# Kernel tuning notes

Measured on AMD Instinct MI355X. Metric: run time of the kernel, lower is better.

## Reference

```python
import jax, jax.numpy as jnp
import numpy as np

H = 2            # attention heads
HID = 128        # hidden_channels
NEG_SLOPE = 0.2  # GATConv leaky_relu slope

N_USER, N_POST, N_ENT = 100000, 50000, 20000
TEXT_D, USER_D, ENT_D = 768, 64, 64
E_PUB, E_REP, E_CON, E_INT, E_FOL = 150000, 300000, 200000, 500000, 500000


def _gat(h_src, h_dst, src, dst, Wsrc, Wdst, asrc, adst, bias):
    """PyG GATConv((-1,-1), C, heads=H, concat=False, add_self_loops=False)."""
    n_dst = h_dst.shape[0]
    C = Wsrc.shape[1] // H
    xs = (h_src @ Wsrc).reshape(-1, H, C)          # [Ns,H,C]
    xd = (h_dst @ Wdst).reshape(-1, H, C)          # [Nd,H,C]
    al_s = jnp.einsum('nhc,hc->nh', xs, asrc)      # [Ns,H]
    al_d = jnp.einsum('nhc,hc->nh', xd, adst)      # [Nd,H]
    e = jax.nn.leaky_relu(al_s[src] + al_d[dst], NEG_SLOPE)   # [E,H]
    m = jax.ops.segment_max(e, dst, num_segments=n_dst)
    m = jnp.where(jnp.isfinite(m), m, 0.0)
    ex = jnp.exp(e - m[dst])
    denom = jax.ops.segment_sum(ex, dst, num_segments=n_dst)
    alpha = ex / (denom[dst] + 1e-16)              # per-dst softmax
    msg = xs[src] * alpha[:, :, None]              # [E,H,C]
    out = jax.ops.segment_sum(msg, dst, num_segments=n_dst)   # [Nd,H,C]
    return out.mean(axis=1) + bias                 # concat=False -> head mean


def setup_inputs() -> dict:
    key = jax.random.key(0)
    ks = jax.random.split(key, 24)
    s = 0.05
    d = {
        'post_cls': jax.random.normal(ks[0], (N_POST, TEXT_D), jnp.float32),
        'user_x': jax.random.normal(ks[1], (N_USER, USER_D), jnp.float32),
        'entity_x': jax.random.normal(ks[2], (N_ENT, ENT_D), jnp.float32),
        'Wpost': jax.random.normal(ks[3], (TEXT_D, HID), jnp.float32) * s,
        'bpost': jnp.zeros((HID,), jnp.float32),
        'Wuser': jax.random.normal(ks[4], (USER_D, HID), jnp.float32) * s,
        'buser': jnp.zeros((HID,), jnp.float32),
        'Went': jax.random.normal(ks[5], (ENT_D, HID), jnp.float32) * s,
        'bent': jnp.zeros((HID,), jnp.float32),
        # 2 layers x 5 relations (publish, repost, contain, interact, follow)
        'gat_Wsrc': jax.random.normal(ks[6], (2, 5, HID, H * HID), jnp.float32) * s,
        'gat_Wdst': jax.random.normal(ks[7], (2, 5, HID, H * HID), jnp.float32) * s,
        'gat_asrc': jax.random.normal(ks[8], (2, 5, H, HID), jnp.float32) * s,
        'gat_adst': jax.random.normal(ks[9], (2, 5, H, HID), jnp.float32) * s,
        'gat_bias': jnp.zeros((2, 5, HID), jnp.float32),
        'Wc1': jax.random.normal(ks[10], (HID, HID // 2), jnp.float32) * s,
        'bc1': jnp.zeros((HID // 2,), jnp.float32),
        'Wc2': jax.random.normal(ks[11], (HID // 2, 1), jnp.float32) * s,
        'bc2': jnp.zeros((1,), jnp.float32),
        'pub_src': jax.random.randint(ks[12], (E_PUB,), 0, N_USER, jnp.int32),
        'pub_dst': jax.random.randint(ks[13], (E_PUB,), 0, N_POST, jnp.int32),
        'rep_src': jax.random.randint(ks[14], (E_REP,), 0, N_USER, jnp.int32),
        'rep_dst': jax.random.randint(ks[15], (E_REP,), 0, N_POST, jnp.int32),
        'con_src': jax.random.randint(ks[16], (E_CON,), 0, N_POST, jnp.int32),
        'con_dst': jax.random.randint(ks[17], (E_CON,), 0, N_ENT, jnp.int32),
        'int_src': jax.random.randint(ks[18], (E_INT,), 0, N_USER, jnp.int32),
        'int_dst': jax.random.randint(ks[19], (E_INT,), 0, N_USER, jnp.int32),
        'fol_src': jax.random.randint(ks[20], (E_FOL,), 0, N_USER, jnp.int32),
        'fol_dst': jax.random.randint(ks[21], (E_FOL,), 0, N_USER, jnp.int32),
    }
    return d


def _forward(post_cls, user_x, entity_x, Wpost, bpost, Wuser, buser, Went, bent,
             gat_Wsrc, gat_Wdst, gat_asrc, gat_adst, gat_bias,
             Wc1, bc1, Wc2, bc2, edges):
    h = {
        'post': post_cls @ Wpost + bpost,
        'user': user_x @ Wuser + buser,
        'entity': entity_x @ Went + bent,
    }
    for l in range(2):
        def g(r, h_src, h_dst, src, dst):
            return _gat(h_src, h_dst, src, dst,
                        gat_Wsrc[l, r], gat_Wdst[l, r],
                        gat_asrc[l, r], gat_adst[l, r], gat_bias[l, r])
        # HeteroConv aggr='sum' over edge types sharing a dst node type
        new_post = (g(0, h['user'], h['post'], edges['pub_src'], edges['pub_dst'])
                    + g(1, h['user'], h['post'], edges['rep_src'], edges['rep_dst']))
        new_ent = g(2, h['post'], h['entity'], edges['con_src'], edges['con_dst'])
        new_user = (g(3, h['user'], h['user'], edges['int_src'], edges['int_dst'])
                    + g(4, h['user'], h['user'], edges['fol_src'], edges['fol_dst']))
        h = {'post': jax.nn.relu(new_post),
             'user': jax.nn.relu(new_user),
             'entity': jax.nn.relu(new_ent)}
    # classifier (dropout inactive at inference)
    z = jax.nn.relu(h['post'] @ Wc1 + bc1)
    out = z @ Wc2 + bc2
    return out.squeeze(-1)   # [n_posts]


def reference(post_cls, user_x, entity_x, Wpost, bpost, Wuser, buser, Went, bent,
              gat_Wsrc, gat_Wdst, gat_asrc, gat_adst, gat_bias,
              Wc1, bc1, Wc2, bc2,
              pub_src, pub_dst, rep_src, rep_dst, con_src, con_dst,
              int_src, int_dst, fol_src, fol_dst):
    edges = dict(pub_src=pub_src, pub_dst=pub_dst, rep_src=rep_src, rep_dst=rep_dst,
                 con_src=con_src, con_dst=con_dst, int_src=int_src, int_dst=int_dst,
                 fol_src=fol_src, fol_dst=fol_dst)
    return _forward(post_cls, user_x, entity_x, Wpost, bpost, Wuser, buser, Went, bent,
                    gat_Wsrc, gat_Wdst, gat_asrc, gat_adst, gat_bias,
                    Wc1, bc1, Wc2, bc2, edges)
```

## Files before the change

kernel.cpp:

```cpp
#include <hip/hip_runtime.h>
#include <cstdint>
#include <cstddef>

#define N_USER 100000
#define N_POST 50000
#define TEXT_D 768
#define USER_D 64
#define E_TOT 1450000
#define N_TOT 300000

typedef unsigned short ushort_t;
typedef float f4v __attribute__((ext_vector_type(4)));
typedef short s8v __attribute__((ext_vector_type(8)));
typedef unsigned short u4v __attribute__((ext_vector_type(4)));
typedef unsigned short u8v __attribute__((ext_vector_type(8)));

__device__ __forceinline__ float leaky(float v) { return v > 0.f ? v : 0.2f * v; }
__device__ __forceinline__ void split_bf(float x, ushort_t& hi, ushort_t& lo) {
  unsigned u = __float_as_uint(x);
  hi = (ushort_t)(u >> 16);
  float r = x - __uint_as_float(u & 0xFFFF0000u);
  lo = (ushort_t)(__float_as_uint(r) >> 16);
}

struct Ptrs4 { const int* p[4]; };

__global__ void wvec_kernel(const float* __restrict__ W, const float* __restrict__ av,
                            float* __restrict__ wv) {
  int b = blockIdx.x;
  int lr = b / 2, h = b % 2;
  const float* Wp = W + ((size_t)lr * 128 * 256) + (size_t)threadIdx.x * 256 + h * 128;
  const float* ap = av + (size_t)(lr * 2 + h) * 128;
  float acc = 0.f;
  for (int c = 0; c < 128; ++c) acc += Wp[c] * ap[c];
  wv[(size_t)(lr * 2 + h) * 128 + threadIdx.x] = acc;
}

__global__ void wt_prep(const float* __restrict__ W, ushort_t* __restrict__ WTh,
                        ushort_t* __restrict__ WTl, int K, int C) {
  int k = blockIdx.x * 256 + threadIdx.x;
  int c = blockIdx.y;
  if (k >= K) return;
  ushort_t h, l;
  split_bf(W[(size_t)k * C + c], h, l);
  WTh[(size_t)c * K + k] = h;
  WTl[(size_t)c * K + k] = l;
}

__global__ void stk_prep(const float* __restrict__ Wa, const float* __restrict__ Wb,
                         ushort_t* __restrict__ STh, ushort_t* __restrict__ STl) {
  int rel = blockIdx.x;
  int c = blockIdx.y;
  int t = threadIdx.x;
  const float* W = rel ? Wb : Wa;
  float v = W[(size_t)(t & 127) * 256 + (size_t)(t >> 7) * 128 + c];
  ushort_t hh, ll;
  split_bf(v, hh, ll);
  size_t idx = (size_t)c * 512 + (size_t)rel * 256 + t;
  STh[idx] = hh;
  STl[idx] = ll;
}

__global__ void bias_sum(const float* __restrict__ gbias, float* __restrict__ BS) {
  int c = threadIdx.x;
  BS[c]       = gbias[0 * 640 + 0 * 128 + c] + gbias[0 * 640 + 1 * 128 + c];
  BS[128 + c] = gbias[0 * 640 + 3 * 128 + c] + gbias[0 * 640 + 4 * 128 + c];
  BS[256 + c] = gbias[1 * 640 + 0 * 128 + c] + gbias[1 * 640 + 1 * 128 + c];
}

template <bool ASPLIT, bool RELU>
__global__ __launch_bounds__(256) void gemm_pipe(const void* __restrict__ Ag,
                                                 const ushort_t* __restrict__ Agl,
                                                 const ushort_t* __restrict__ Bgh,
                                                 const ushort_t* __restrict__ Bgl,
                                                 const float* __restrict__ bv,
                                                 float* __restrict__ Out,
                                                 int N, int K) {
  __shared__ ushort_t LAh[2][64 * 40], LAl[2][64 * 40];
  __shared__ ushort_t LBh[2][128 * 40], LBl[2][128 * 40];
  int t = threadIdx.x;
  int lane = t & 63, w = t >> 6;
  int m = lane & 15, quad = lane >> 4;
  int wr = w >> 1, wc = w & 1;
  int row0 = blockIdx.x * 64;
  int nkb = K >> 5;

  const float* Xf = (const float*)Ag;
  const ushort_t* Xh = (const ushort_t*)Ag;

  int arf[2], af4[2];
  int ars = 0, ags = 0;
  if (!ASPLIT) {
#pragma unroll
    for (int i = 0; i < 2; ++i) {
      int p = t + 256 * i;
      int r = p >> 3;
      int row = row0 + r;
      arf[i] = (row < N) ? row : (N - 1);
      af4[i] = p & 7;
    }
  } else {
    int r = t >> 2;
    int row = row0 + r;
    ars = (row < N) ? row : (N - 1);
    ags = t & 3;
  }
  int bc_[2], bg_[2];
#pragma unroll
  for (int i = 0; i < 2; ++i) {
    int p = t + 256 * i;
    bc_[i] = p >> 2;
    bg_[i] = p & 3;
  }

  f4v acc[2][4];
#pragma unroll
  for (int mt = 0; mt < 2; ++mt)
#pragma unroll
    for (int ct = 0; ct < 4; ++ct) acc[mt][ct] = (f4v){0.f, 0.f, 0.f, 0.f};

  float4 pa0[2], pa1[2];
  u8v pah0, pal0, pah1, pal1;
  u8v pbh0[2], pbl0[2], pbh1[2], pbl1[2];

#define LOADG(S, KB)                                                          \
  do {                                                                        \
    int k0 = (KB) * 32;                                                       \
    if (ASPLIT) {                                                             \
      pah##S = *(const u8v*)(Xh + (size_t)ars * K + k0 + ags * 8);            \
      pal##S = *(const u8v*)(Agl + (size_t)ars * K + k0 + ags * 8);           \
    } else {                                                                  \
      _Pragma("unroll")                                                       \
      for (int i = 0; i < 2; ++i)                                             \
        pa##S[i] = *(const float4*)(Xf + (size_t)arf[i] * K + k0 + af4[i] * 4);\
    }                                                                         \
    _Pragma("unroll")                                                         \
    for (int i = 0; i < 2; ++i) {                                             \
      pbh##S[i] = *(const u8v*)(Bgh + (size_t)bc_[i] * K + k0 + bg_[i] * 8);  \
      pbl##S[i] = *(const u8v*)(Bgl + (size_t)bc_[i] * K + k0 + bg_[i] * 8);  \
    }                                                                         \
  } while (0)

#define WRITES(S)                                                             \
  do {                                                                        \
    if (ASPLIT) {                                                             \
      int r = t >> 2, g = t & 3;                                              \
      *(u8v*)&LAh[S][r * 40 + g * 8] = pah##S;                                \
      *(u8v*)&LAl[S][r * 40 + g * 8] = pal##S;                                \
    } else {                                                                  \
      _Pragma("unroll")                                                       \
      for (int i = 0; i < 2; ++i) {                                           \
        int p = t + 256 * i;                                                  \
        int r = p >> 3, f4i = p & 7;                                          \
        u4v hh, ll;                                                           \
        ushort_t sh, sl;                                                      \
        split_bf(pa##S[i].x, sh, sl); hh[0] = sh; ll[0] = sl;                 \
        split_bf(pa##S[i].y, sh, sl); hh[1] = sh; ll[1] = sl;                 \
        split_bf(pa##S[i].z, sh, sl); hh[2] = sh; ll[2] = sl;                 \
        split_bf(pa##S[i].w, sh, sl); hh[3] = sh; ll[3] = sl;                 \
        *(u4v*)&LAh[S][r * 40 + f4i * 4] = hh;                                \
        *(u4v*)&LAl[S][r * 40 + f4i * 4] = ll;                                \
      }                                                                       \
    }                                                                         \
    _Pragma("unroll")                                                         \
    for (int i = 0; i < 2; ++i) {                                             \
      int c = bc_[i], g = bg_[i];                                             \
      *(u8v*)&LBh[S][c * 40 + g * 8] = pbh##S[i];                             \
      *(u8v*)&LBl[S][c * 40 + g * 8] = pbl##S[i];                             \
    }                                                                         \
  } while (0)

  auto MF = [&](int buf) {
    s8v ah[2], al2[2];
#pragma unroll
    for (int mt = 0; mt < 2; ++mt) {
      int r = wr * 32 + mt * 16 + m;
      ah[mt] = *(const s8v*)&LAh[buf][r * 40 + quad * 8];
      al2[mt] = *(const s8v*)&LAl[buf][r * 40 + quad * 8];
    }
#pragma unroll
    for (int ct = 0; ct < 4; ++ct) {
      int c = wc * 64 + ct * 16 + m;
      s8v bh = *(const s8v*)&LBh[buf][c * 40 + quad * 8];
      s8v bl = *(const s8v*)&LBl[buf][c * 40 + quad * 8];
#pragma unroll
      for (int mt = 0; mt < 2; ++mt) {
        acc[mt][ct] = __builtin_amdgcn_mfma_f32_16x16x32_bf16(ah[mt], bh, acc[mt][ct], 0, 0, 0);
        acc[mt][ct] = __builtin_amdgcn_mfma_f32_16x16x32_bf16(ah[mt], bl, acc[mt][ct], 0, 0, 0);
        acc[mt][ct] = __builtin_amdgcn_mfma_f32_16x16x32_bf16(al2[mt], bh, acc[mt][ct], 0, 0, 0);
      }
    }
  };

  LOADG(0, 0);
  if (nkb > 1) LOADG(1, 1);
  int kb = 0;
  for (; kb + 2 <= nkb; kb += 2) {
    WRITES(0);
    __syncthreads();
    if (kb + 2 < nkb) LOADG(0, kb + 2);
    MF(0);
    WRITES(1);
    __syncthreads();
    if (kb + 3 < nkb) LOADG(1, kb + 3);
    MF(1);
  }
  if (kb < nkb) {
    WRITES(0);
    __syncthreads();
    MF(0);
  }
#undef LOADG
#undef WRITES

  float bb[4];
#pragma unroll
  for (int ct = 0; ct < 4; ++ct) bb[ct] = bv[wc * 64 + ct * 16 + m];
#pragma unroll
  for (int mt = 0; mt < 2; ++mt)
#pragma unroll
    for (int j = 0; j < 4; ++j) {
      int row = row0 + wr * 32 + mt * 16 + quad * 4 + j;
      if (row < N) {
        float* o = Out + (size_t)row * 128 + wc * 64 + m;
#pragma unroll
        for (int ct = 0; ct < 4; ++ct) {
          float vv = acc[mt][ct][j] + bb[ct];
          if (RELU) vv = fmaxf(vv, 0.f);
          o[ct * 16] = vv;
        }
      }
    }
}

__device__ __forceinline__ void rel_of(int g, int& r, int& loc, int& nb) {
  if (g < 450000) {
    if (g < 150000) { r = 0; loc = g;          nb = 0; }
    else            { r = 1; loc = g - 150000; nb = 50000; }
  } else if (g < 950000)  { r = 2; loc = g - 450000;  nb = 100000; }
  else                    { r = 3; loc = g - 950000;  nb = 200000; }
}
__global__ void histc_kernel(Ptrs4 dsts, int* __restrict__ cnt) {
  int g = blockIdx.x * 256 + threadIdx.x;
  if (g >= E_TOT) return;
  int r, loc, nb;
  rel_of(g, r, loc, nb);
  atomicAdd(&cnt[nb + dsts.p[r][loc]], 1);
}
__global__ __launch_bounds__(256) void scan1_kernel(const int* __restrict__ cnt,
                                                    int* __restrict__ excl,
                                                    int* __restrict__ partials, int Nd) {
  __shared__ int sb[256];
  int t = threadIdx.x;
  int base = blockIdx.x * 1024 + t * 4;
  int v[4];
#pragma unroll
  for (int j = 0; j < 4; ++j) v[j] = (base + j < Nd) ? cnt[base + j] : 0;
  int tot = v[0] + v[1] + v[2] + v[3];
  sb[t] = tot;
  __syncthreads();
  for (int off = 1; off < 256; off <<= 1) {
    int x = 0;
    if (t >= off) x = sb[t - off];
    __syncthreads();
    sb[t] += x;
    __syncthreads();
  }
  int ex = sb[t] - tot;
  if (t == 255) partials[blockIdx.x] = sb[t];
  int run = ex;
#pragma unroll
  for (int j = 0; j < 4; ++j) {
    if (base + j < Nd) excl[base + j] = run;
    run += v[j];
  }
}
__global__ __launch_bounds__(512) void scan2_kernel(int* __restrict__ partials, int B) {
  __shared__ int sb[512];
  int t = threadIdx.x;
  int v = (t < B) ? partials[t] : 0;
  sb[t] = v;
  __syncthreads();
  for (int off = 1; off < 512; off <<= 1) {
    int x = 0;
    if (t >= off) x = sb[t - off];
    __syncthreads();
    sb[t] += x;
    __syncthreads();
  }
  if (t < B) partials[t] = sb[t] - v;
}
__global__ void scan3_kernel(const int* __restrict__ excl, const int* __restrict__ partials,
                             int* __restrict__ rowptr, int* __restrict__ cursor) {
  int i = blockIdx.x * 256 + threadIdx.x;
  if (i < N_TOT) {
    int v = excl[i] + partials[i >> 10];
    rowptr[i] = v;
    cursor[i] = v;
  }
  if (i == 0) rowptr[N_TOT] = E_TOT;
}
__global__ void scatterc_kernel(Ptrs4 srcs, Ptrs4 dsts,
                                int* __restrict__ cursor, int* __restrict__ csrc) {
  int g = blockIdx.x * 256 + threadIdx.x;
  if (g >= E_TOT) return;
  int r, loc, nb;
  rel_of(g, r, loc, nb);
  int p = atomicAdd(&cursor[nb + dsts.p[r][loc]], 1);
  csrc[p] = srcs.p[r][loc];
}

__global__ __launch_bounds__(256) void logits2_kernel(const float* __restrict__ H,
                                                      const float* __restrict__ wsA,
                                                      const float* __restrict__ wsB,
                                                      float* __restrict__ alsA,
                                                      float* __restrict__ alsB, int Ns) {
  int n = blockIdx.x * 4 + (threadIdx.x >> 6);
  int lane = threadIdx.x & 63;
  if (n >= Ns) return;
  const float* hr = H + (size_t)n * 128;
  float ha = hr[lane], hb = hr[lane + 64];
  float p0 = ha * wsA[lane] + hb * wsA[lane + 64];
  float p1 = ha * wsA[128 + lane] + hb * wsA[192 + lane];
  float p2 = ha * wsB[lane] + hb * wsB[lane + 64];
  float p3 = ha * wsB[128 + lane] + hb * wsB[192 + lane];
#pragma unroll
  for (int mk = 32; mk; mk >>= 1) {
    p0 += __shfl_xor(p0, mk); p1 += __shfl_xor(p1, mk);
    p2 += __shfl_xor(p2, mk); p3 += __shfl_xor(p3, mk);
  }
  if (lane == 0) {
    *(float2*)(alsA + 2 * (size_t)n) = make_float2(p0, p1);
    *(float2*)(alsB + 2 * (size_t)n) = make_float2(p2, p3);
  }
}

__global__ __launch_bounds__(256) void aggG2_kernel(const int* __restrict__ rowA,
                                                    const int* __restrict__ rowB,
                                                    const int* __restrict__ csrc,
                                                    const float* __restrict__ alsA,
                                                    const float* __restrict__ alsB,
                                                    const float* __restrict__ wdvA,
                                                    const float* __restrict__ wdvB,
                                                    const float* __restrict__ Hs,
                                                    const float* __restrict__ Hd,
                                                    ushort_t* __restrict__ Gh,
                                                    ushort_t* __restrict__ Gl,
                                                    int Nd, int dOff) {
  int w = threadIdx.x >> 6;
  int lane = threadIdx.x & 63;
  int rel = w & 1;
  int hw = lane >> 5, s = lane & 31;
  int dl = blockIdx.x * 4 + (w >> 1) * 2 + hw;
  if (dl >= Nd) return;
  int d = dl + dOff;
  const int* rp = rel ? rowB : rowA;
  const float* als = rel ? alsB : alsA;
  const float* wdv = rel ? wdvB : wdvA;

  const float* hr = Hd + (size_t)d * 128;
  float t0 = 0.f, t1 = 0.f;
#pragma unroll
  for (int j = 0; j < 4; ++j) {
    float hv = hr[s + 32 * j];
    t0 += hv * wdv[s + 32 * j];
    t1 += hv * wdv[128 + s + 32 * j];
  }
#pragma unroll
  for (int mk = 16; mk; mk >>= 1) { t0 += __shfl_xor(t0, mk); t1 += __shfl_xor(t1, mk); }

  int start = rp[d], end = rp[d + 1];
  float den0 = 0.f, den1 = 0.f;
  f4v a0 = (f4v){0.f, 0.f, 0.f, 0.f}, a1 = (f4v){0.f, 0.f, 0.f, 0.f};
  if (end > start) {
    int last = end - 1;
    for (int b0 = start; b0 < end; b0 += 8) {
      int sid[8]; bool vl[8];
#pragma unroll
      for (int j = 0; j < 8; ++j) {
        int ee = b0 + j;
        vl[j] = ee < end;
        sid[j] = csrc[vl[j] ? ee : last];
      }
      float2 al[8]; f4v x[8];
#pragma unroll
      for (int j = 0; j < 8; ++j) {
        al[j] = *(const float2*)(als + 2 * (size_t)sid[j]);
        x[j] = *(const f4v*)(Hs + (size_t)sid[j] * 128 + 4 * s);
      }
#pragma unroll
      for (int j = 0; j < 8; ++j) {
        float w0 = vl[j] ? __expf(leaky(al[j].x + t0)) : 0.f;
        float w1 = vl[j] ? __expf(leaky(al[j].y + t1)) : 0.f;
        den0 += w0; den1 += w1;
#pragma unroll
        for (int q = 0; q < 4; ++q) { a0[q] += w0 * x[j][q]; a1[q] += w1 * x[j][q]; }
      }
    }
  }
  float i0 = 0.5f / (den0 + 1e-16f);
  float i1 = 0.5f / (den1 + 1e-16f);
  ushort_t* gh = Gh + (size_t)dl * 512 + rel * 256;
  ushort_t* gl = Gl + (size_t)dl * 512 + rel * 256;
  u4v g0h, g0l, g1h, g1l;
#pragma unroll
  for (int q = 0; q < 4; ++q) {
    ushort_t hh, ll;
    split_bf(a0[q] * i0, hh, ll); g0h[q] = hh; g0l[q] = ll;
    split_bf(a1[q] * i1, hh, ll); g1h[q] = hh; g1l[q] = ll;
  }
  *(u4v*)(gh + 4 * s) = g0h;
  *(u4v*)(gl + 4 * s) = g0l;
  *(u4v*)(gh + 128 + 4 * s) = g1h;
  *(u4v*)(gl + 128 + 4 * s) = g1l;
}

__global__ __launch_bounds__(256) void classifier_kernel(const float* __restrict__ Hp,
                                                         const float* __restrict__ Wc1, const float* __restrict__ bc1,
                                                         const float* __restrict__ Wc2, const float* __restrict__ bc2,
                                                         float* __restrict__ out, int N) {
  __shared__ float sW[128 * 64];
  int t = threadIdx.x;
#pragma unroll
  for (int i = 0; i < 8; ++i) ((float4*)sW)[t + 256 * i] = ((const float4*)Wc1)[t + 256 * i];
  __syncthreads();
  int lane = t & 63, wv = t >> 6;
  float b = bc1[lane], w2 = Wc2[lane], b2 = bc2[0];
#pragma unroll
  for (int nn = 0; nn < 2; ++nn) {
    int n = blockIdx.x * 8 + wv * 2 + nn;
    if (n >= N) continue;
    const float* hr = Hp + (size_t)n * 128;
    float accz = b;
    for (int k = 0; k < 128; ++k) accz += hr[k] * sW[k * 64 + lane];
    float z = fmaxf(accz, 0.f) * w2;
#pragma unroll
    for (int off = 32; off; off >>= 1) z += __shfl_down(z, off);
    if (lane == 0) out[n] = z + b2;
  }
}

extern "C" void kernel_launch(void* const* d_in, const int* in_sizes, int n_in,
                              void* d_out, int out_size, void* d_ws, size_t ws_size,
                              hipStream_t stream) {
  const float* post_cls = (const float*)d_in[0];
  const float* user_x   = (const float*)d_in[1];
  const float* Wpost = (const float*)d_in[3];
  const float* bpost = (const float*)d_in[4];
  const float* Wuser = (const float*)d_in[5];
  const float* buser = (const float*)d_in[6];
  const float* gWsrc = (const float*)d_in[9];
  const float* gWdst = (const float*)d_in[10];
  const float* gasrc = (const float*)d_in[11];
  const float* gadst = (const float*)d_in[12];
  const float* gbias = (const float*)d_in[13];
  const float* Wc1 = (const float*)d_in[14];
  const float* bc1 = (const float*)d_in[15];
  const float* Wc2 = (const float*)d_in[16];
  const float* bc2 = (const float*)d_in[17];
  Ptrs4 SRCS, DSTS;
  SRCS.p[0] = (const int*)d_in[18]; DSTS.p[0] = (const int*)d_in[19];
  SRCS.p[1] = (const int*)d_in[20]; DSTS.p[1] = (const int*)d_in[21];
  SRCS.p[2] = (const int*)d_in[24]; DSTS.p[2] = (const int*)d_in[25];
  SRCS.p[3] = (const int*)d_in[26]; DSTS.p[3] = (const int*)d_in[27];
  float* out = (float*)d_out;
  (void)ws_size; (void)in_sizes; (void)n_in; (void)out_size;

  float* Wf = (float*)d_ws;
  size_t o = 0;
  float* WDSTV = Wf + o; o += 2560;
  float* WSRCV = Wf + o; o += 2560;
  float* BS    = Wf + o; o += 384;
  float* ALSa  = Wf + o; o += (size_t)N_USER * 2;
  float* ALSb  = Wf + o; o += (size_t)N_USER * 2;
  float* HU    = Wf + o; o += (size_t)N_USER * 128;
  float* HP    = Wf + o; o += (size_t)N_POST * 128;
  float* TMP   = Wf + o; o += (size_t)N_POST * 128;
  int* Wi = (int*)(Wf + o);
  size_t io = 0;
  int* RP   = Wi + io; io += N_TOT + 1;
  int* CURS = Wi + io; io += N_TOT;
  int* CNT  = Wi + io; io += N_TOT;
  int* EXCL = Wi + io; io += N_TOT;
  int* PART = Wi + io; io += 512;
  int* CSRC = Wi + io; io += E_TOT;
  io = (io + 7) & ~(size_t)7;
  ushort_t* Wu = (ushort_t*)(Wi + io);
  size_t uo = 0;
  ushort_t* PWh = Wu + uo; uo += 128 * TEXT_D;
  ushort_t* PWl = Wu + uo; uo += 128 * TEXT_D;
  ushort_t* UWh = Wu + uo; uo += 128 * USER_D;
  ushort_t* UWl = Wu + uo; uo += 128 * USER_D;
  ushort_t* STh[3]; ushort_t* STl[3];
  for (int i = 0; i < 3; ++i) {
    STh[i] = Wu + uo; uo += 128 * 512;
    STl[i] = Wu + uo; uo += 128 * 512;
  }
  ushort_t* Gh = Wu + uo; uo += (size_t)N_POST * 512;
  ushort_t* Gl = Wu + uo; uo += (size_t)N_POST * 512;

  const int NOFF_PUB = 0, NOFF_REP = 50000, NOFF_INT = 100000, NOFF_FOL = 200000;

  (void)hipMemsetAsync(CNT, 0, (size_t)N_TOT * sizeof(int), stream);
  histc_kernel<<<(E_TOT + 255) / 256, 256, 0, stream>>>(DSTS, CNT);
  int B = (N_TOT + 1023) / 1024;
  scan1_kernel<<<B, 256, 0, stream>>>(CNT, EXCL, PART, N_TOT);
  scan2_kernel<<<1, 512, 0, stream>>>(PART, B);
  scan3_kernel<<<(N_TOT + 255) / 256, 256, 0, stream>>>(EXCL, PART, RP, CURS);
  scatterc_kernel<<<(E_TOT + 255) / 256, 256, 0, stream>>>(SRCS, DSTS, CURS, CSRC);

  wt_prep<<<dim3(3, 128), 256, 0, stream>>>(Wpost, PWh, PWl, TEXT_D, 128);
  wt_prep<<<dim3(1, 128), 256, 0, stream>>>(Wuser, UWh, UWl, USER_D, 128);
  stk_prep<<<dim3(2, 128), 256, 0, stream>>>(gWsrc + (size_t)0 * 32768, gWsrc + (size_t)1 * 32768, STh[0], STl[0]);
  stk_prep<<<dim3(2, 128), 256, 0, stream>>>(gWsrc + (size_t)3 * 32768, gWsrc + (size_t)4 * 32768, STh[1], STl[1]);
  stk_prep<<<dim3(2, 128), 256, 0, stream>>>(gWsrc + (size_t)5 * 32768, gWsrc + (size_t)6 * 32768, STh[2], STl[2]);
  wvec_kernel<<<20, 128, 0, stream>>>(gWdst, gadst, WDSTV);
  wvec_kernel<<<20, 128, 0, stream>>>(gWsrc, gasrc, WSRCV);
  bias_sum<<<1, 128, 0, stream>>>(gbias, BS);

  gemm_pipe<false, false><<<(N_POST + 63) / 64, 256, 0, stream>>>(
      post_cls, nullptr, PWh, PWl, bpost, HP, N_POST, TEXT_D);
  gemm_pipe<false, false><<<(N_USER + 63) / 64, 256, 0, stream>>>(
      user_x, nullptr, UWh, UWl, buser, HU, N_USER, USER_D);

  logits2_kernel<<<(N_USER + 3) / 4, 256, 0, stream>>>(
      HU, WSRCV + 0 * 256, WSRCV + 1 * 256, ALSa, ALSb, N_USER);
  aggG2_kernel<<<(N_POST + 3) / 4, 256, 0, stream>>>(
      RP + NOFF_PUB, RP + NOFF_REP, CSRC, ALSa, ALSb,
      WDSTV + 0 * 256, WDSTV + 1 * 256, HU, HP, Gh, Gl, N_POST, 0);
  gemm_pipe<true, true><<<(N_POST + 63) / 64, 256, 0, stream>>>(
      Gh, Gl, STh[0], STl[0], BS + 0, HP, N_POST, 512);

  logits2_kernel<<<(N_USER + 3) / 4, 256, 0, stream>>>(
      HU, WSRCV + 3 * 256, WSRCV + 4 * 256, ALSa, ALSb, N_USER);
  aggG2_kernel<<<(50000 + 3) / 4, 256, 0, stream>>>(
      RP + NOFF_INT, RP + NOFF_FOL, CSRC, ALSa, ALSb,
      WDSTV + 3 * 256, WDSTV + 4 * 256, HU, HU, Gh, Gl, 50000, 0);
  gemm_pipe<true, true><<<(50000 + 63) / 64, 256, 0, stream>>>(
      Gh, Gl, STh[1], STl[1], BS + 128, TMP, 50000, 512);
  aggG2_kernel<<<(50000 + 3) / 4, 256, 0, stream>>>(
      RP + NOFF_INT, RP + NOFF_FOL, CSRC, ALSa, ALSb,
      WDSTV + 3 * 256, WDSTV + 4 * 256, HU, HU, Gh, Gl, 50000, 50000);
  gemm_pipe<true, true><<<(50000 + 63) / 64, 256, 0, stream>>>(
      Gh, Gl, STh[1], STl[1], BS + 128, HU + (size_t)50000 * 128, 50000, 512);
  (void)hipMemcpyAsync(HU, TMP, (size_t)50000 * 128 * sizeof(float),
                       hipMemcpyDeviceToDevice, stream);

  logits2_kernel<<<(N_USER + 3) / 4, 256, 0, stream>>>(
      HU, WSRCV + 5 * 256, WSRCV + 6 * 256, ALSa, ALSb, N_USER);
  aggG2_kernel<<<(N_POST + 3) / 4, 256, 0, stream>>>(
      RP + NOFF_PUB, RP + NOFF_REP, CSRC, ALSa, ALSb,
      WDSTV + 5 * 256, WDSTV + 6 * 256, HU, HP, Gh, Gl, N_POST, 0);
  gemm_pipe<true, true><<<(N_POST + 63) / 64, 256, 0, stream>>>(
      Gh, Gl, STh[2], STl[2], BS + 256, HP, N_POST, 512);

  classifier_kernel<<<(N_POST + 7) / 8, 256, 0, stream>>>(HP, Wc1, bc1, Wc2, bc2, out, N_POST);
}
```

Before: 1.125 ms.

## Load GEMM MFMA operands straight from global memory, dropping LDS staging

The split-bf16 MFMA GEMM no longer stages A and B tiles through double-buffered shared memory with barriers. Each lane now loads its MFMA fragments directly from global memory into registers, using a two-stage register prefetch, and does the fp32 hi/lo split in registers. This removes the LDS writes, reads and __syncthreads. In exchange, B tiles are loaded redundantly by every wave, the global access pattern becomes less coalesced (16-byte reads strided by row), and register pressure rises.

```diff
diff --git a/kernel.cpp b/kernel.cpp
--- a/kernel.cpp
+++ b/kernel.cpp
@@ -13,7 +13,6 @@
 typedef float f4v __attribute__((ext_vector_type(4)));
 typedef short s8v __attribute__((ext_vector_type(8)));
 typedef unsigned short u4v __attribute__((ext_vector_type(4)));
-typedef unsigned short u8v __attribute__((ext_vector_type(8)));
 
 __device__ __forceinline__ float leaky(float v) { return v > 0.f ? v : 0.2f * v; }
 __device__ __forceinline__ void split_bf(float x, ushort_t& hi, ushort_t& lo) {
@@ -69,49 +68,29 @@
 }
 
 template <bool ASPLIT, bool RELU>
-__global__ __launch_bounds__(256) void gemm_pipe(const void* __restrict__ Ag,
-                                                 const ushort_t* __restrict__ Agl,
-                                                 const ushort_t* __restrict__ Bgh,
-                                                 const ushort_t* __restrict__ Bgl,
-                                                 const float* __restrict__ bv,
-                                                 float* __restrict__ Out,
-                                                 int N, int K) {
-  __shared__ ushort_t LAh[2][64 * 40], LAl[2][64 * 40];
-  __shared__ ushort_t LBh[2][128 * 40], LBl[2][128 * 40];
+__global__ __launch_bounds__(256) void gemm_direct(const void* __restrict__ Ag,
+                                                   const ushort_t* __restrict__ Agl,
+                                                   const ushort_t* __restrict__ Bgh,
+                                                   const ushort_t* __restrict__ Bgl,
+                                                   const float* __restrict__ bv,
+                                                   float* __restrict__ Out,
+                                                   int N, int K) {
   int t = threadIdx.x;
   int lane = t & 63, w = t >> 6;
   int m = lane & 15, quad = lane >> 4;
   int wr = w >> 1, wc = w & 1;
   int row0 = blockIdx.x * 64;
-  int nkb = K >> 5;
+  int nks = K >> 5;
 
   const float* Xf = (const float*)Ag;
   const ushort_t* Xh = (const ushort_t*)Ag;
 
-  int arf[2], af4[2];
-  int ars = 0, ags = 0;
-  if (!ASPLIT) {
-#pragma unroll
-    for (int i = 0; i < 2; ++i) {
-      int p = t + 256 * i;
-      int r = p >> 3;
-      int row = row0 + r;
-      arf[i] = (row < N) ? row : (N - 1);
-      af4[i] = p & 7;
-    }
-  } else {
-    int r = t >> 2;
-    int row = row0 + r;
-    ars = (row < N) ? row : (N - 1);
-    ags = t & 3;
-  }
-  int bc_[2], bg_[2];
-#pragma unroll
-  for (int i = 0; i < 2; ++i) {
-    int p = t + 256 * i;
-    bc_[i] = p >> 2;
-    bg_[i] = p & 3;
-  }
+  int r0 = row0 + wr * 32 + m;       if (r0 >= N) r0 = N - 1;
+  int r1 = row0 + wr * 32 + 16 + m;  if (r1 >= N) r1 = N - 1;
+  size_t a0 = (size_t)r0 * K, a1 = (size_t)r1 * K;
+  size_t bbase[4];
+#pragma unroll
+  for (int ct = 0; ct < 4; ++ct) bbase[ct] = (size_t)(wc * 64 + ct * 16 + m) * K;
 
   f4v acc[2][4];
 #pragma unroll
@@ -119,99 +98,78 @@
 #pragma unroll
     for (int ct = 0; ct < 4; ++ct) acc[mt][ct] = (f4v){0.f, 0.f, 0.f, 0.f};
 
-  float4 pa0[2], pa1[2];
-  u8v pah0, pal0, pah1, pal1;
-  u8v pbh0[2], pbl0[2], pbh1[2], pbl1[2];
-
-#define LOADG(S, KB)                                                          \
+  s8v a0h0, a0l0, a1h0, a1l0, a0h1, a0l1, a1h1, a1l1;
+  float4 f0a0, f0b0, f1a0, f1b0, f0a1, f0b1, f1a1, f1b1;
+  s8v bh0[4], bl0[4], bh1[4], bl1[4];
+
+#define LOADD(S, KS)                                                          \
   do {                                                                        \
-    int k0 = (KB) * 32;                                                       \
-    if (ASPLIT) {                                                             \
-      pah##S = *(const u8v*)(Xh + (size_t)ars * K + k0 + ags * 8);            \
-      pal##S = *(const u8v*)(Agl + (size_t)ars * K + k0 + ags * 8);           \
+    int koff = (KS) * 32 + quad * 8;                                          \
+    if constexpr (ASPLIT) {                                                   \
+      a0h##S = *(const s8v*)(Xh + a0 + koff);                                 \
+      a0l##S = *(const s8v*)(Agl + a0 + koff);                                \
+      a1h##S = *(const s8v*)(Xh + a1 + koff);                                 \
+      a1l##S = *(const s8v*)(Agl + a1 + koff);                                \
     } else {                                                                  \
-      _Pragma("unroll")                                                       \
-      for (int i = 0; i < 2; ++i)                                             \
-        pa##S[i] = *(const float4*)(Xf + (size_t)arf[i] * K + k0 + af4[i] * 4);\
+      f0a##S = *(const float4*)(Xf + a0 + koff);                              \
+      f0b##S = *(const float4*)(Xf + a0 + koff + 4);                          \
+      f1a##S = *(const float4*)(Xf + a1 + koff);                              \
+      f1b##S = *(const float4*)(Xf + a1 + koff + 4);                          \
     }                                                                         \
     _Pragma("unroll")                                                         \
-    for (int i = 0; i < 2; ++i) {                                             \
-      pbh##S[i] = *(const u8v*)(Bgh + (size_t)bc_[i] * K + k0 + bg_[i] * 8);  \
-      pbl##S[i] = *(const u8v*)(Bgl + (size_t)bc_[i] * K + k0 + bg_[i] * 8);  \
+    for (int ct = 0; ct < 4; ++ct) {                                          \
+      bh##S[ct] = *(const s8v*)(Bgh + bbase[ct] + koff);                      \
+      bl##S[ct] = *(const s8v*)(Bgl + bbase[ct] + koff);                      \
     }                                                                         \
   } while (0)
 
-#define WRITES(S)                                                             \
+#define MFMAD(S)                                                              \
   do {                                                                        \
-    if (ASPLIT) {                                                             \
-      int r = t >> 2, g = t & 3;                                              \
-      *(u8v*)&LAh[S][r * 40 + g * 8] = pah##S;                                \
-      *(u8v*)&LAl[S][r * 40 + g * 8] = pal##S;                                \
+    s8v ah0_, al0_, ah1_, al1_;                                               \
+    if constexpr (ASPLIT) {                                                   \
+      ah0_ = a0h##S; al0_ = a0l##S; ah1_ = a1h##S; al1_ = a1l##S;             \
     } else {                                                                  \
-      _Pragma("unroll")                                                       \
-      for (int i = 0; i < 2; ++i) {                                           \
-        int p = t + 256 * i;                                                  \
-        int r = p >> 3, f4i = p & 7;                                          \
-        u4v hh, ll;                                                           \
-        ushort_t sh, sl;                                                      \
-        split_bf(pa##S[i].x, sh, sl); hh[0] = sh; ll[0] = sl;                 \
-        split_bf(pa##S[i].y, sh, sl); hh[1] = sh; ll[1] = sl;                 \
-        split_bf(pa##S[i].z, sh, sl); hh[2] = sh; ll[2] = sl;                 \
-        split_bf(pa##S[i].w, sh, sl); hh[3] = sh; ll[3] = sl;                 \
-        *(u4v*)&LAh[S][r * 40 + f4i * 4] = hh;                                \
-        *(u4v*)&LAl[S][r * 40 + f4i * 4] = ll;                                \
-      }                                                                       \
+      ushort_t sh, sl;                                                        \
+      split_bf(f0a##S.x, sh, sl); ah0_[0] = (short)sh; al0_[0] = (short)sl;   \
+      split_bf(f0a##S.y, sh, sl); ah0_[1] = (short)sh; al0_[1] = (short)sl;   \
+      split_bf(f0a##S.z, sh, sl); ah0_[2] = (short)sh; al0_[2] = (short)sl;   \
+      split_bf(f0a##S.w, sh, sl); ah0_[3] = (short)sh; al0_[3] = (short)sl;   \
+      split_bf(f0b##S.x, sh, sl); ah0_[4] = (short)sh; al0_[4] = (short)sl;   \
+      split_bf(f0b##S.y, sh, sl); ah0_[5] = (short)sh; al0_[5] = (short)sl;   \
+      split_bf(f0b##S.z, sh, sl); ah0_[6] = (short)sh; al0_[6] = (short)sl;   \
+      split_bf(f0b##S.w, sh, sl); ah0_[7] = (short)sh; al0_[7] = (short)sl;   \
+      split_bf(f1a##S.x, sh, sl); ah1_[0] = (short)sh; al1_[0] = (short)sl;   \
+      split_bf(f1a##S.y, sh, sl); ah1_[1] = (short)sh; al1_[1] = (short)sl;   \
+      split_bf(f1a##S.z, sh, sl); ah1_[2] = (short)sh; al1_[2] = (short)sl;   \
+      split_bf(f1a##S.w, sh, sl); ah1_[3] = (short)sh; al1_[3] = (short)sl;   \
+      split_bf(f1b##S.x, sh, sl); ah1_[4] = (short)sh; al1_[4] = (short)sl;   \
+      split_bf(f1b##S.y, sh, sl); ah1_[5] = (short)sh; al1_[5] = (short)sl;   \
+      split_bf(f1b##S.z, sh, sl); ah1_[6] = (short)sh; al1_[6] = (short)sl;   \
+      split_bf(f1b##S.w, sh, sl); ah1_[7] = (short)sh; al1_[7] = (short)sl;   \
     }                                                                         \
     _Pragma("unroll")                                                         \
-    for (int i = 0; i < 2; ++i) {                                             \
-      int c = bc_[i], g = bg_[i];                                             \
-      *(u8v*)&LBh[S][c * 40 + g * 8] = pbh##S[i];                             \
-      *(u8v*)&LBl[S][c * 40 + g * 8] = pbl##S[i];                             \
+    for (int ct = 0; ct < 4; ++ct) {                                          \
+      s8v bh_ = bh##S[ct], bl_ = bl##S[ct];                                   \
+      acc[0][ct] = __builtin_amdgcn_mfma_f32_16x16x32_bf16(ah0_, bh_, acc[0][ct], 0, 0, 0); \
+      acc[0][ct] = __builtin_amdgcn_mfma_f32_16x16x32_bf16(ah0_, bl_, acc[0][ct], 0, 0, 0); \
+      acc[0][ct] = __builtin_amdgcn_mfma_f32_16x16x32_bf16(al0_, bh_, acc[0][ct], 0, 0, 0); \
+      acc[1][ct] = __builtin_amdgcn_mfma_f32_16x16x32_bf16(ah1_, bh_, acc[1][ct], 0, 0, 0); \
+      acc[1][ct] = __builtin_amdgcn_mfma_f32_16x16x32_bf16(ah1_, bl_, acc[1][ct], 0, 0, 0); \
+      acc[1][ct] = __builtin_amdgcn_mfma_f32_16x16x32_bf16(al1_, bh_, acc[1][ct], 0, 0, 0); \
     }                                                                         \
   } while (0)
 
-  auto MF = [&](int buf) {
-    s8v ah[2], al2[2];
-#pragma unroll
-    for (int mt = 0; mt < 2; ++mt) {
-      int r = wr * 32 + mt * 16 + m;
-      ah[mt] = *(const s8v*)&LAh[buf][r * 40 + quad * 8];
-      al2[mt] = *(const s8v*)&LAl[buf][r * 40 + quad * 8];
-    }
-#pragma unroll
-    for (int ct = 0; ct < 4; ++ct) {
-      int c = wc * 64 + ct * 16 + m;
-      s8v bh = *(const s8v*)&LBh[buf][c * 40 + quad * 8];
-      s8v bl = *(const s8v*)&LBl[buf][c * 40 + quad * 8];
-#pragma unroll
-      for (int mt = 0; mt < 2; ++mt) {
-        acc[mt][ct] = __builtin_amdgcn_mfma_f32_16x16x32_bf16(ah[mt], bh, acc[mt][ct], 0, 0, 0);
-        acc[mt][ct] = __builtin_amdgcn_mfma_f32_16x16x32_bf16(ah[mt], bl, acc[mt][ct], 0, 0, 0);
-        acc[mt][ct] = __builtin_amdgcn_mfma_f32_16x16x32_bf16(al2[mt], bh, acc[mt][ct], 0, 0, 0);
-      }
-    }
-  };
-
-  LOADG(0, 0);
-  if (nkb > 1) LOADG(1, 1);
-  int kb = 0;
-  for (; kb + 2 <= nkb; kb += 2) {
-    WRITES(0);
-    __syncthreads();
-    if (kb + 2 < nkb) LOADG(0, kb + 2);
-    MF(0);
-    WRITES(1);
-    __syncthreads();
-    if (kb + 3 < nkb) LOADG(1, kb + 3);
-    MF(1);
-  }
-  if (kb < nkb) {
-    WRITES(0);
-    __syncthreads();
-    MF(0);
-  }
-#undef LOADG
-#undef WRITES
+  LOADD(0, 0);
+  int ks = 0;
+  for (; ks + 2 <= nks; ks += 2) {
+    LOADD(1, ks + 1);
+    MFMAD(0);
+    if (ks + 2 < nks) LOADD(0, ks + 2);
+    MFMAD(1);
+  }
+  if (ks < nks) MFMAD(0);
+#undef LOADD
+#undef MFMAD
 
   float bb[4];
 #pragma unroll
@@ -518,9 +476,9 @@
   wvec_kernel<<<20, 128, 0, stream>>>(gWsrc, gasrc, WSRCV);
   bias_sum<<<1, 128, 0, stream>>>(gbias, BS);
 
-  gemm_pipe<false, false><<<(N_POST + 63) / 64, 256, 0, stream>>>(
+  gemm_direct<false, false><<<(N_POST + 63) / 64, 256, 0, stream>>>(
       post_cls, nullptr, PWh, PWl, bpost, HP, N_POST, TEXT_D);
-  gemm_pipe<false, false><<<(N_USER + 63) / 64, 256, 0, stream>>>(
+  gemm_direct<false, false><<<(N_USER + 63) / 64, 256, 0, stream>>>(
       user_x, nullptr, UWh, UWl, buser, HU, N_USER, USER_D);
 
   logits2_kernel<<<(N_USER + 3) / 4, 256, 0, stream>>>(
@@ -528,7 +486,7 @@
   aggG2_kernel<<<(N_POST + 3) / 4, 256, 0, stream>>>(
       RP + NOFF_PUB, RP + NOFF_REP, CSRC, ALSa, ALSb,
       WDSTV + 0 * 256, WDSTV + 1 * 256, HU, HP, Gh, Gl, N_POST, 0);
-  gemm_pipe<true, true><<<(N_POST + 63) / 64, 256, 0, stream>>>(
+  gemm_direct<true, true><<<(N_POST + 63) / 64, 256, 0, stream>>>(
       Gh, Gl, STh[0], STl[0], BS + 0, HP, N_POST, 512);
 
   logits2_kernel<<<(N_USER + 3) / 4, 256, 0, stream>>>(
@@ -536,12 +494,12 @@
   aggG2_kernel<<<(50000 + 3) / 4, 256, 0, stream>>>(
       RP + NOFF_INT, RP + NOFF_FOL, CSRC, ALSa, ALSb,
       WDSTV + 3 * 256, WDSTV + 4 * 256, HU, HU, Gh, Gl, 50000, 0);
-  gemm_pipe<true, true><<<(50000 + 63) / 64, 256, 0, stream>>>(
+  gemm_direct<true, true><<<(50000 + 63) / 64, 256, 0, stream>>>(
       Gh, Gl, STh[1], STl[1], BS + 128, TMP, 50000, 512);
   aggG2_kernel<<<(50000 + 3) / 4, 256, 0, stream>>>(
       RP + NOFF_INT, RP + NOFF_FOL, CSRC, ALSa, ALSb,
       WDSTV + 3 * 256, WDSTV + 4 * 256, HU, HU, Gh, Gl, 50000, 50000);
-  gemm_pipe<true, true><<<(50000 + 63) / 64, 256, 0, stream>>>(
+  gemm_direct<true, true><<<(50000 + 63) / 64, 256, 0, stream>>>(
       Gh, Gl, STh[1], STl[1], BS + 128, HU + (size_t)50000 * 128, 50000, 512);
   (void)hipMemcpyAsync(HU, TMP, (size_t)50000 * 128 * sizeof(float),
                        hipMemcpyDeviceToDevice, stream);
@@ -551,7 +509,7 @@
   aggG2_kernel<<<(N_POST + 3) / 4, 256, 0, stream>>>(
       RP + NOFF_PUB, RP + NOFF_REP, CSRC, ALSa, ALSb,
       WDSTV + 5 * 256, WDSTV + 6 * 256, HU, HP, Gh, Gl, N_POST, 0);
-  gemm_pipe<true, true><<<(N_POST + 63) / 64, 256, 0, stream>>>(
+  gemm_direct<true, true><<<(N_POST + 63) / 64, 256, 0, stream>>>(
       Gh, Gl, STh[2], STl[2], BS + 256, HP, N_POST, 512);
 
   classifier_kernel<<<(N_POST + 7) / 8, 256, 0, stream>>>(HP, Wc1, bc1, Wc2, bc2, out, N_POST);
```

Result: slower. 1.372 ms (+22.0%).
